# Kernel tuning notes

Measured on AMD Instinct MI355X. Metric: run time of the kernel, lower is better.

## Reference

```python
import jax, jax.numpy as jnp
import numpy as np

B, N, K, D_IN, D, L = 8, 8192, 6, 3, 256, 5
EPS_LN = 1e-5


def layernorm(x, g, b):
    m = jnp.mean(x, axis=-1, keepdims=True)
    v = jnp.mean((x - m) ** 2, axis=-1, keepdims=True)
    return (x - m) * jax.lax.rsqrt(v + EPS_LN) * g + b


def spmm_mean(v, knn):
    # sparse adj matmul: out[j] = sum_{n: j in knn[n]} v[n], then / k
    n, k = knn.shape[-2], knn.shape[-1]
    src = jnp.repeat(jnp.arange(n), k)  # [N*K]

    def one(vb, kb):
        return jnp.zeros_like(vb).at[kb.reshape(-1)].add(vb[src])

    return jax.vmap(one)(v, knn) / (k + 1e-6)


def grf_layer(h, knn, qkv_w, out_w, out_b, hops=3):
    q, k, v = jnp.split(h @ qkv_w, 3, axis=-1)
    for _ in range(hops):
        v = spmm_mean(v, knn)
        k = spmm_mean(k, knn)
    attn = jnp.sum(q * k, axis=-1, keepdims=True)
    return (attn * v) @ out_w + out_b


def linear_attention(h, qkv_w, out_w, out_b):
    q, k, v = jnp.split(h @ qkv_w, 3, axis=-1)
    q = jax.nn.relu(q) + 1e-6
    k = jax.nn.relu(k) + 1e-6
    kv = jnp.einsum('bnd,bne->bde', k, v)
    z = 1.0 / (jnp.einsum('bnd,bd->bn', q, k.sum(axis=1)) + 1e-6)
    attn = jnp.einsum('bnd,bde,bn->bne', q, kv, z)
    return attn @ out_w + out_b


def setup_inputs() -> dict:
    key = jax.random.key(0)
    ks = jax.random.split(key, 12)
    s = 0.02
    return {
        'x': jax.random.normal(ks[0], (B, N, D_IN), jnp.float32),
        'knn': jax.random.randint(ks[1], (B, N, K), 0, N, jnp.int32),
        'emb_w': jax.random.normal(ks[2], (D_IN, D), jnp.float32) * s,
        'emb_b': jnp.zeros((D,), jnp.float32),
        'norm_g': jnp.ones((2 * L, D), jnp.float32),
        'norm_b': jnp.zeros((2 * L, D), jnp.float32),
        'grf_qkv': jax.random.normal(ks[3], (L, D, 3 * D), jnp.float32) * s,
        'grf_outw': jax.random.normal(ks[4], (L, D, D), jnp.float32) * s,
        'grf_outb': jnp.zeros((L, D), jnp.float32),
        'attn_qkv': jax.random.normal(ks[5], (L, D, 3 * D), jnp.float32) * s,
        'attn_outw': jax.random.normal(ks[6], (L, D, D), jnp.float32) * s,
        'attn_outb': jnp.zeros((L, D), jnp.float32),
        'head_w': jax.random.normal(ks[7], (D, 3), jnp.float32) * s,
        'head_b': jnp.zeros((3,), jnp.float32),
    }


def reference(x, knn, emb_w, emb_b, norm_g, norm_b, grf_qkv, grf_outw, grf_outb,
              attn_qkv, attn_outw, attn_outb, head_w, head_b):
    h = x @ emb_w + emb_b
    for i in range(L):
        h = h + grf_layer(layernorm(h, norm_g[2 * i], norm_b[2 * i]), knn,
                          grf_qkv[i], grf_outw[i], grf_outb[i])
        h = h + linear_attention(layernorm(h, norm_g[2 * i + 1], norm_b[2 * i + 1]),
                                 attn_qkv[i], attn_outw[i], attn_outb[i])
    return h @ head_w + head_b
```

## Files before the change

kernel.cpp:

```cpp
#include <hip/hip_runtime.h>

#define BB 8
#define NN 8192
#define KK 6
#define DD 256
#define LL 5
#define NE (BB*NN*KK)
#define PLANE (NN*DD)
#define INV6 (1.0f/6.000001f)

typedef unsigned short u16;
typedef __attribute__((ext_vector_type(8))) _Float16 h8;
typedef __attribute__((ext_vector_type(8))) unsigned short us8;
typedef __attribute__((ext_vector_type(4))) float f32x4;

__device__ __forceinline__ u16 f2h(float f){
  union { _Float16 h; u16 u; } c; c.h = (_Float16)f; return c.u;
}
__device__ __forceinline__ float h2f(u16 u){
  union { _Float16 h; u16 u; } c; c.u = u; return (float)c.h;
}

__device__ __forceinline__ void ldscp(const u16* g, u16* l){
  __builtin_amdgcn_global_load_lds(
      (const __attribute__((address_space(1))) void*)g,
      (__attribute__((address_space(3))) void*)l, 16, 0, 0);
}

__global__ void k_count(const int* __restrict__ knn, int* __restrict__ off){
  int e = blockIdx.x*256 + threadIdx.x;
  if(e >= NE) return;
  int b = e / (NN*KK);
  int j = knn[e];
  atomicAdd(&off[b*(NN+1) + 1 + j], 1);
}

__global__ __launch_bounds__(1024) void k_scan(int* __restrict__ offAll){
  __shared__ int lds[1024];
  __shared__ int carry_s;
  int* off = offAll + blockIdx.x*(NN+1);
  const int len = NN+1;
  int t = threadIdx.x;
  if(t==0) carry_s = 0;
  __syncthreads();
  for(int base=0; base<len; base+=1024){
    int x = (base+t < len) ? off[base+t] : 0;
    lds[t] = x; __syncthreads();
    for(int s=1; s<1024; s<<=1){
      int v = (t>=s) ? lds[t-s] : 0;
      __syncthreads();
      lds[t] += v;
      __syncthreads();
    }
    int incl = lds[t];
    int carry = carry_s;
    __syncthreads();
    if(base+t < len) off[base+t] = incl + carry;
    if(t==1023) carry_s = carry + incl;
    __syncthreads();
  }
}

__global__ void k_fill(const int* __restrict__ knn, int* __restrict__ cursor, int* __restrict__ srcE){
  int e = blockIdx.x*256 + threadIdx.x;
  if(e >= NE) return;
  int b = e / (NN*KK);
  int n = (e % (NN*KK)) / KK;
  int j = knn[e];
  int pos = atomicAdd(&cursor[b*(NN+1) + j], 1);
  srcE[(long)b*NN*KK + pos] = n;
}

__global__ __launch_bounds__(256) void k_prepw(const float* __restrict__ W, u16* __restrict__ Wt, int N){
  int n = blockIdx.x, l = blockIdx.y, k = threadIdx.x;
  float x = W[((long)l*256 + k)*N + n];
  u16 hb = f2h(x);
  Wt[(((long)l*2 + 0)*N + n)*256 + k] = hb;
  Wt[(((long)l*2 + 1)*N + n)*256 + k] = f2h(x - h2f(hb));
}

__global__ __launch_bounds__(256) void k_embed(const float* __restrict__ x, const float* __restrict__ ew,
                        const float* __restrict__ eb, float* __restrict__ h){
  int g = blockIdx.x, z = blockIdx.y, d = threadIdx.x;
  const float* xp = x + ((long)z*NN + g)*3;
  h[(long)z*PLANE + (long)g*DD + d] = xp[0]*ew[0*DD+d] + xp[1]*ew[1*DD+d] + xp[2]*ew[2*DD+d] + eb[d];
}

__global__ __launch_bounds__(256) void k_ln(const float* __restrict__ h, const float* __restrict__ g,
                     const float* __restrict__ bia, u16* __restrict__ out){
  long z = blockIdx.y;
  int row = blockIdx.x*4 + (threadIdx.x >> 6);
  int lane = threadIdx.x & 63;
  const float4 x = *(const float4*)(h + z*PLANE + (long)row*DD + lane*4);
  float s  = x.x + x.y + x.z + x.w;
  float s2 = x.x*x.x + x.y*x.y + x.z*x.z + x.w*x.w;
  for(int o=1;o<64;o<<=1){ s += __shfl_xor(s,o); s2 += __shfl_xor(s2,o); }
  float m = s*(1.0f/256.0f);
  float var = s2*(1.0f/256.0f) - m*m;
  float r = rsqrtf(var + 1e-5f);
  const float4 gu = *(const float4*)(g + lane*4);
  const float4 bu = *(const float4*)(bia + lane*4);
  ushort4 o4;
  o4.x = f2h((x.x-m)*r*gu.x + bu.x);
  o4.y = f2h((x.y-m)*r*gu.y + bu.y);
  o4.z = f2h((x.z-m)*r*gu.z + bu.z);
  o4.w = f2h((x.w-m)*r*gu.w + bu.w);
  *(ushort4*)(out + z*PLANE + (long)row*DD + lane*4) = o4;
}

template<int BM,int BN,bool ASPLIT,bool BF32,bool BSPLIT>
__global__ __launch_bounds__(256) void k_mgemm(
    const u16* __restrict__ A, long aStride, long aLoOff, int K, int kSplit,
    const void* __restrict__ Bv, long bStride, long bLoOff,
    const float* __restrict__ rowscale, long rsStride,
    const float* __restrict__ bias,
    u16* __restrict__ o0, u16* __restrict__ o1, u16* __restrict__ o2,
    long oStride, int reluMask, long oLoOff,
    float* __restrict__ accOut, long hStride)
{
  constexpr int WM = BM/2, WN = BN/2, MT = WM/16, NT = WN/16;
  constexpr int STG1 = BM*32*(ASPLIT?2:1) + BN*32*(BSPLIT?2:1);
  constexpr int STGT = BF32 ? STG1 : 2*STG1;
  constexpr int EPI = (BM==128) ? 32*132*2 : 0;
  constexpr int SM  = (STGT > EPI) ? STGT : EPI;
  __shared__ __align__(16) u16 smem[SM];
  float* epi = (float*)smem;

  const int t = threadIdx.x;
  const int nz = blockIdx.z;
  const long z = nz / kSplit;
  const int chunk = nz % kSplit;
  const int kLen = K / kSplit, kLo = chunk * kLen;
  const int rowTile = blockIdx.x*BM, colTile = blockIdx.y*BN;
  const int l = t & 63, w = t >> 6;
  const int wr = w >> 1, wc = w & 1;
  const int lm = l & 15, kq = l >> 4;

  f32x4 acc[MT][NT];
  #pragma unroll
  for(int mt=0;mt<MT;mt++)
    #pragma unroll
    for(int nt=0;nt<NT;nt++) acc[mt][nt] = (f32x4){0.f,0.f,0.f,0.f};

  if constexpr (!BF32){
    auto stageAB = [&](int buf, int k0){
      u16* Ahi_ = smem + (size_t)buf*STG1;
      u16* Alo_ = Ahi_ + BM*32;
      u16* Bhi_ = Ahi_ + BM*32*(ASPLIT?2:1);
      u16* Blo_ = Bhi_ + BN*32;
      {
        constexpr int NCH = BM/64;
        #pragma unroll
        for(int li=0; li<NCH; li++){
          int f = li*256 + t;
          int row = f>>2, c = (f&3)*8;
          const u16* gp = A + z*aStride + (long)(rowTile+row)*K + k0 + c;
          ldscp(gp, &Ahi_[f*8]);
          if constexpr (ASPLIT) ldscp(gp + aLoOff, &Alo_[f*8]);
        }
      }
      {
        constexpr int NCH = BN/64;
        #pragma unroll
        for(int li=0; li<NCH; li++){
          int f = li*256 + t;
          int row = f>>2, c = (f&3)*8;
          const u16* gp = (const u16*)Bv + z*bStride + (long)(colTile+row)*K + k0 + c;
          ldscp(gp, &Bhi_[f*8]);
          if constexpr (BSPLIT) ldscp(gp + bLoOff, &Blo_[f*8]);
        }
      }
    };

    const int nsteps = kLen >> 5;
    stageAB(0, kLo);
    __syncthreads();
    int cur = 0;
    for(int ks=0; ks<nsteps; ++ks){
      if(ks+1 < nsteps) stageAB(cur^1, kLo + ((ks+1)<<5));
      const u16* Ahi_ = smem + (size_t)cur*STG1;
      const u16* Alo_ = Ahi_ + BM*32;
      const u16* Bhi_ = Ahi_ + BM*32*(ASPLIT?2:1);
      const u16* Blo_ = Bhi_ + BN*32;
      h8 ah[MT], al[MT], bh[NT], bl[NT];
      #pragma unroll
      for(int mt=0;mt<MT;mt++){
        int idx = (wr*WM + mt*16 + lm)*32 + kq*8;
        ah[mt] = *(const h8*)&Ahi_[idx];
        if constexpr (ASPLIT) al[mt] = *(const h8*)&Alo_[idx];
      }
      #pragma unroll
      for(int nt=0;nt<NT;nt++){
        int idx = (wc*WN + nt*16 + lm)*32 + kq*8;
        bh[nt] = *(const h8*)&Bhi_[idx];
        if constexpr (BSPLIT) bl[nt] = *(const h8*)&Blo_[idx];
      }
      #pragma unroll
      for(int mt=0;mt<MT;mt++)
        #pragma unroll
        for(int nt=0;nt<NT;nt++){
          acc[mt][nt] = __builtin_amdgcn_mfma_f32_16x16x32_f16(ah[mt], bh[nt], acc[mt][nt], 0, 0, 0);
          if constexpr (BSPLIT)
            acc[mt][nt] = __builtin_amdgcn_mfma_f32_16x16x32_f16(ah[mt], bl[nt], acc[mt][nt], 0, 0, 0);
          if constexpr (ASPLIT)
            acc[mt][nt] = __builtin_amdgcn_mfma_f32_16x16x32_f16(al[mt], bh[nt], acc[mt][nt], 0, 0, 0);
        }
      __syncthreads();
      cur ^= 1;
    }
  } else {
    u16* Ahi = smem;
    u16* Alo = smem + BM*32;
    u16* Bhi = smem + BM*32*(ASPLIT?2:1);
    for(int k0=kLo; k0<kLo+kLen; k0+=32){
      __syncthreads();
      {
        constexpr int NCH = BM/64;
        #pragma unroll
        for(int li=0; li<NCH; li++){
          int f = li*256 + t;
          int row = f>>2, c = (f&3)*8;
          const u16* gp = A + z*aStride + (long)(rowTile+row)*K + k0 + c;
          ldscp(gp, &Ahi[f*8]);
          if constexpr (ASPLIT) ldscp(gp + aLoOff, &Alo[f*8]);
        }
      }
      {
        constexpr int NCH = BN/64;
        #pragma unroll
        for(int li=0; li<NCH; li++){
          int f = li*256 + t;
          int row = f>>2, c = (f&3)*8;
          const float* src = (const float*)Bv + z*bStride + (long)(colTile+row)*K + k0 + c;
          float4 v0 = ((const float4*)src)[0], v1 = ((const float4*)src)[1];
          us8 hv;
          hv[0]=f2h(v0.x); hv[1]=f2h(v0.y); hv[2]=f2h(v0.z); hv[3]=f2h(v0.w);
          hv[4]=f2h(v1.x); hv[5]=f2h(v1.y); hv[6]=f2h(v1.z); hv[7]=f2h(v1.w);
          *(us8*)&Bhi[f*8] = hv;
        }
      }
      __syncthreads();
      h8 ah[MT], al[MT], bh[NT];
      #pragma unroll
      for(int mt=0;mt<MT;mt++){
        int idx = (wr*WM + mt*16 + lm)*32 + kq*8;
        ah[mt] = *(const h8*)&Ahi[idx];
        if constexpr (ASPLIT) al[mt] = *(const h8*)&Alo[idx];
      }
      #pragma unroll
      for(int nt=0;nt<NT;nt++){
        int idx = (wc*WN + nt*16 + lm)*32 + kq*8;
        bh[nt] = *(const h8*)&Bhi[idx];
      }
      #pragma unroll
      for(int mt=0;mt<MT;mt++)
        #pragma unroll
        for(int nt=0;nt<NT;nt++){
          acc[mt][nt] = __builtin_amdgcn_mfma_f32_16x16x32_f16(ah[mt], bh[nt], acc[mt][nt], 0, 0, 0);
          if constexpr (ASPLIT)
            acc[mt][nt] = __builtin_amdgcn_mfma_f32_16x16x32_f16(al[mt], bh[nt], acc[mt][nt], 0, 0, 0);
        }
    }
  }

  if constexpr (BM == 128){
    const int sec = colTile >> 8;
    u16* osec = (sec==0) ? o0 : ((sec==1) ? o1 : o2);
    const bool relu = (reluMask >> sec) & 1;
    #pragma unroll
    for(int mt=0;mt<MT;mt++){
      __syncthreads();
      #pragma unroll
      for(int r=0;r<4;r++){
        int gm = rowTile + wr*64 + mt*16 + kq*4 + r;
        float sc = rowscale ? rowscale[z*rsStride + gm] : 1.0f;
        int rl = wr*16 + kq*4 + r;
        #pragma unroll
        for(int nt=0;nt<NT;nt++)
          epi[rl*132 + wc*64 + nt*16 + lm] = acc[mt][nt][r]*sc;
      }
      __syncthreads();
      #pragma unroll
      for(int ss=0;ss<2;ss++){
        int s = ss*256 + t;
        int rl = s >> 4, sc8 = (s & 15)*8;
        int gm2 = rowTile + (rl>>4)*64 + mt*16 + (rl & 15);
        float v[8];
        #pragma unroll
        for(int j=0;j<8;j++) v[j] = epi[rl*132 + sc8 + j];
        if(bias){
          const float* bp = bias + colTile + sc8;
          #pragma unroll
          for(int j=0;j<8;j++) v[j] += bp[j];
        }
        if(accOut){
          float* hp = accOut + z*hStride + (long)gm2*256 + colTile + sc8;
          float4 h0 = ((float4*)hp)[0], h1 = ((float4*)hp)[1];
          h0.x += v[0]; h0.y += v[1]; h0.z += v[2]; h0.w += v[3];
          h1.x += v[4]; h1.y += v[5]; h1.z += v[6]; h1.w += v[7];
          ((float4*)hp)[0] = h0; ((float4*)hp)[1] = h1;
        } else {
          us8 o8;
          #pragma unroll
          for(int j=0;j<8;j++){
            float vv = v[j];
            if(relu) vv = fmaxf(vv, 0.f) + 1e-6f;
            o8[j] = f2h(vv);
          }
          *(us8*)(osec + z*oStride + (long)gm2*256 + ((colTile + sc8) & 255)) = o8;
        }
      }
    }
  } else {
    #pragma unroll
    for(int mt=0;mt<MT;mt++){
      #pragma unroll
      for(int r=0;r<4;r++){
        int gm = rowTile + wr*WM + mt*16 + kq*4 + r;
        float sc = rowscale ? rowscale[z*rsStride + gm] : 1.0f;
        if(accOut){
          float* hp = accOut + z*hStride + (long)gm*256;
          if(kSplit > 1){
            #pragma unroll
            for(int nt=0;nt<NT;nt++){
              int gc = colTile + wc*WN + nt*16 + lm;
              atomicAdd(&hp[gc], acc[mt][nt][r]);
            }
          } else {
            #pragma unroll
            for(int nt=0;nt<NT;nt++){
              int gc = colTile + wc*WN + nt*16 + lm;
              hp[gc] += acc[mt][nt][r]*sc + (bias ? bias[gc] : 0.f);
            }
          }
        } else {
          #pragma unroll
          for(int nt=0;nt<NT;nt++){
            int gc = colTile + wc*WN + nt*16 + lm;
            int sec = gc >> 8;
            u16* o = (sec==0) ? o0 : ((sec==1) ? o1 : o2);
            float val = acc[mt][nt][r]*sc + (bias ? bias[gc] : 0.f);
            if((reluMask >> sec) & 1) val = fmaxf(val, 0.f) + 1e-6f;
            if(sec==0 && oLoOff){
              u16* oo = o0 + 2*z*oStride + (long)gm*256 + (gc & 255);
              u16 hb = f2h(val);
              oo[0] = hb;
              oo[oLoOff] = f2h(val - h2f(hb));
            } else {
              o[z*oStride + (long)gm*256 + (gc & 255)] = f2h(val);
            }
          }
        }
      }
    }
  }
}

__global__ __launch_bounds__(256) void k_fusedout(
    const u16* __restrict__ A, const u16* __restrict__ B, long bStride, long bLoOff,
    const float* __restrict__ rowscale, const float* __restrict__ ksumIn,
    const float* __restrict__ bias,
    float* __restrict__ h,
    const float* __restrict__ lnG, const float* __restrict__ lnB,
    u16* __restrict__ Lout,
    const float* __restrict__ headW, const float* __restrict__ headB,
    float* __restrict__ headOut)
{
  __shared__ __align__(16) u16 smem[16384];
  u16* Bh = smem;
  u16* Bl = smem + 8192;
  float* epi = (float*)smem;

  const int t = threadIdx.x;
  const long z = blockIdx.z;
  const int rowTile = blockIdx.x*32;
  const int l = t & 63, w = t >> 6;
  const int wr = w >> 1, wc = w & 1;
  const int lm = l & 15, kq = l >> 4;
  const u16* Ab = A + z*PLANE;
  const u16* Bb = B + z*bStride;

  f32x4 acc[8];
  #pragma unroll
  for(int nt=0;nt<8;nt++) acc[nt] = (f32x4){0.f,0.f,0.f,0.f};

  h8 areg[8];
  {
    const u16* arow = Ab + (long)(rowTile + wr*16 + lm)*256 + kq*8;
    #pragma unroll
    for(int kk=0;kk<8;kk++) areg[kk] = *(const h8*)(arow + kk*32);
  }

  float rsv = 0.f;
  if(ksumIn){
    const float* kb = ksumIn + z*DD;
    float s = 0.f;
    #pragma unroll
    for(int kk=0;kk<8;kk++){
      const float4 c0v = *(const float4*)(kb + kq*8 + kk*32);
      const float4 c1v = *(const float4*)(kb + kq*8 + kk*32 + 4);
      s += (float)areg[kk][0]*c0v.x + (float)areg[kk][1]*c0v.y
         + (float)areg[kk][2]*c0v.z + (float)areg[kk][3]*c0v.w
         + (float)areg[kk][4]*c1v.x + (float)areg[kk][5]*c1v.y
         + (float)areg[kk][6]*c1v.z + (float)areg[kk][7]*c1v.w;
    }
    s += __shfl_xor(s, 16);
    s += __shfl_xor(s, 32);
    rsv = 1.0f/(s + 1e-6f);
  }

  #pragma unroll
  for(int kk=0; kk<8; ++kk){
    __syncthreads();
    #pragma unroll
    for(int li=0; li<4; li++){
      int f = li*256 + t;
      int row = f>>2, c = (f&3)*8;
      const u16* gp = Bb + (long)row*256 + kk*32 + c;
      ldscp(gp, &Bh[f*8]);
      ldscp(gp + bLoOff, &Bl[f*8]);
    }
    __syncthreads();
    #pragma unroll
    for(int nt=0;nt<8;nt++){
      int idx = (wc*128 + nt*16 + lm)*32 + kq*8;
      const h8 bhf = *(const h8*)&Bh[idx];
      const h8 blf = *(const h8*)&Bl[idx];
      acc[nt] = __builtin_amdgcn_mfma_f32_16x16x32_f16(areg[kk], bhf, acc[nt], 0, 0, 0);
      acc[nt] = __builtin_amdgcn_mfma_f32_16x16x32_f16(areg[kk], blf, acc[nt], 0, 0, 0);
    }
  }

  #pragma unroll
  for(int p=0;p<2;p++){
    __syncthreads();
    if(wr == p){
      #pragma unroll
      for(int r=0;r<4;r++){
        int rl = kq*4 + r;
        int gm = rowTile + p*16 + rl;
        float sc;
        if(ksumIn) sc = __shfl(rsv, kq*4 + r);
        else       sc = rowscale ? rowscale[z*NN + gm] : 1.0f;
        #pragma unroll
        for(int nt=0;nt<8;nt++)
          epi[rl*260 + wc*128 + nt*16 + lm] = acc[nt][r]*sc;
      }
    }
    __syncthreads();
    #pragma unroll
    for(int ss=0;ss<4;ss++){
      int s = ss*256 + t;
      int rl = s >> 6;
      int c4 = (s & 63)*4;
      int gm = rowTile + p*16 + rl;
      float4 e = *(float4*)&epi[rl*260 + c4];
      float4 x;
      x.x = e.x + bias[c4+0];
      x.y = e.y + bias[c4+1];
      x.z = e.z + bias[c4+2];
      x.w = e.w + bias[c4+3];
      float* hp = h + z*PLANE + (long)gm*256 + c4;
      float4 h0 = *(float4*)hp;
      x.x += h0.x; x.y += h0.y; x.z += h0.z; x.w += h0.w;
      *(float4*)hp = x;
      if(lnG){
        float sA = x.x + x.y + x.z + x.w;
        float s2 = x.x*x.x + x.y*x.y + x.z*x.z + x.w*x.w;
        for(int o=1;o<64;o<<=1){ sA += __shfl_xor(sA,o); s2 += __shfl_xor(s2,o); }
        float m = sA*(1.0f/256.0f);
        float var = s2*(1.0f/256.0f) - m*m;
        float rr = rsqrtf(var + 1e-5f);
        const float4 gu = *(const float4*)(lnG + c4);
        const float4 bu = *(const float4*)(lnB + c4);
        ushort4 o4;
        o4.x = f2h((x.x-m)*rr*gu.x + bu.x);
        o4.y = f2h((x.y-m)*rr*gu.y + bu.y);
        o4.z = f2h((x.z-m)*rr*gu.z + bu.z);
        o4.w = f2h((x.w-m)*rr*gu.w + bu.w);
        *(ushort4*)(Lout + z*PLANE + (long)gm*256 + c4) = o4;
      } else if(headW){
        int d0 = c4;
        float a0 = x.x*headW[(d0+0)*3+0] + x.y*headW[(d0+1)*3+0] + x.z*headW[(d0+2)*3+0] + x.w*headW[(d0+3)*3+0];
        float a1 = x.x*headW[(d0+0)*3+1] + x.y*headW[(d0+1)*3+1] + x.z*headW[(d0+2)*3+1] + x.w*headW[(d0+3)*3+1];
        float a2 = x.x*headW[(d0+0)*3+2] + x.y*headW[(d0+1)*3+2] + x.z*headW[(d0+2)*3+2] + x.w*headW[(d0+3)*3+2];
        for(int o=1;o<64;o<<=1){
          a0 += __shfl_xor(a0,o); a1 += __shfl_xor(a1,o); a2 += __shfl_xor(a2,o);
        }
        if((t & 63)==0){
          float* op = headOut + ((long)z*NN + gm)*3;
          op[0] = a0 + headB[0];
          op[1] = a1 + headB[1];
          op[2] = a2 + headB[2];
        }
      }
    }
  }
}

template<int MODE>
__global__ __launch_bounds__(256) void k_spmm2(
    const u16* __restrict__ kin, const u16* __restrict__ vin,
    const int* __restrict__ offB, const int* __restrict__ srcB,
    u16* __restrict__ kout, u16* __restrict__ vout,
    const u16* __restrict__ q, float* __restrict__ rs){
  long z = blockIdx.x;
  const int* off = offB + z*(NN+1);
  const int* sE  = srcB + z*(long)NN*KK;

  if constexpr (MODE == 0){
    const u16* kp = kin + z*PLANE;
    const u16* vp = vin + z*PLANE;
    int row = blockIdx.y*16 + (threadIdx.x >> 4);
    int d8 = blockIdx.z*128 + (threadIdx.x & 15)*8;
    int s0 = off[row], s1 = off[row+1];
    float ak[8], av[8];
    #pragma unroll
    for(int j=0;j<8;j++){ ak[j]=0.f; av[j]=0.f; }
    int e = s0;
    for(; e+1 < s1; e += 2){
      int n0 = sE[e], n1 = sE[e+1];
      us8 k0 = *(const us8*)(kp + (long)n0*DD + d8);
      us8 k1 = *(const us8*)(kp + (long)n1*DD + d8);
      us8 v0 = *(const us8*)(vp + (long)n0*DD + d8);
      us8 v1 = *(const us8*)(vp + (long)n1*DD + d8);
      #pragma unroll
      for(int j=0;j<8;j++){
        ak[j] += h2f(k0[j]) + h2f(k1[j]);
        av[j] += h2f(v0[j]) + h2f(v1[j]);
      }
    }
    if(e < s1){
      int n0 = sE[e];
      us8 k0 = *(const us8*)(kp + (long)n0*DD + d8);
      us8 v0 = *(const us8*)(vp + (long)n0*DD + d8);
      #pragma unroll
      for(int j=0;j<8;j++){ ak[j] += h2f(k0[j]); av[j] += h2f(v0[j]); }
    }
    us8 ok, ov;
    #pragma unroll
    for(int j=0;j<8;j++){ ok[j] = f2h(ak[j]*INV6); ov[j] = f2h(av[j]*INV6); }
    *(us8*)(kout + z*PLANE + (long)row*DD + d8) = ok;
    *(us8*)(vout + z*PLANE + (long)row*DD + d8) = ov;
  } else {
    if(blockIdx.z == 0){
      const u16* kp = kin + z*PLANE;
      int row = blockIdx.y*8 + (threadIdx.x >> 5);
      int l32 = threadIdx.x & 31;
      int d8 = l32*8;
      int s0 = off[row], s1 = off[row+1];
      float ak[8];
      #pragma unroll
      for(int j=0;j<8;j++) ak[j]=0.f;
      int e = s0;
      for(; e+1 < s1; e += 2){
        int n0 = sE[e], n1 = sE[e+1];
        us8 k0 = *(const us8*)(kp + (long)n0*DD + d8);
        us8 k1 = *(const us8*)(kp + (long)n1*DD + d8);
        #pragma unroll
        for(int j=0;j<8;j++) ak[j] += h2f(k0[j]) + h2f(k1[j]);
      }
      if(e < s1){
        int n0 = sE[e];
        us8 k0 = *(const us8*)(kp + (long)n0*DD + d8);
        #pragma unroll
        for(int j=0;j<8;j++) ak[j] += h2f(k0[j]);
      }
      us8 qv = *(const us8*)(q + z*PLANE + (long)row*DD + d8);
      float s = 0.f;
      #pragma unroll
      for(int j=0;j<8;j++) s += h2f(qv[j]) * ak[j];
      for(int o=1;o<32;o<<=1) s += __shfl_xor(s,o);
      if(l32==0) rs[z*NN + row] = s*INV6;
    } else {
      const u16* vp = vin + z*PLANE;
      int row = (blockIdx.y & 511)*16 + (threadIdx.x >> 4);
      int d8 = (blockIdx.y >> 9)*128 + (threadIdx.x & 15)*8;
      int s0 = off[row], s1 = off[row+1];
      float av[8];
      #pragma unroll
      for(int j=0;j<8;j++) av[j]=0.f;
      int e = s0;
      for(; e+1 < s1; e += 2){
        int n0 = sE[e], n1 = sE[e+1];
        us8 v0 = *(const us8*)(vp + (long)n0*DD + d8);
        us8 v1 = *(const us8*)(vp + (long)n1*DD + d8);
        #pragma unroll
        for(int j=0;j<8;j++) av[j] += h2f(v0[j]) + h2f(v1[j]);
      }
      if(e < s1){
        int n0 = sE[e];
        us8 v0 = *(const us8*)(vp + (long)n0*DD + d8);
        #pragma unroll
        for(int j=0;j<8;j++) av[j] += h2f(v0[j]);
      }
      us8 ov;
      #pragma unroll
      for(int j=0;j<8;j++) ov[j] = f2h(av[j]*INV6);
      *(us8*)(vout + z*PLANE + (long)row*DD + d8) = ov;
    }
  }
}

__global__ __launch_bounds__(256) void k_transp2(
    const u16* __restrict__ in0, u16* __restrict__ out0,
    const u16* __restrict__ in1, u16* __restrict__ out1,
    float* __restrict__ ksum){
  __shared__ u16 tile[64][72];
  int zz = blockIdx.z;
  long z = zz >> 1;
  const u16* ip = ((zz & 1) ? in1 : in0) + z*PLANE;
  u16* op = ((zz & 1) ? out1 : out0) + z*PLANE;
  int r0 = blockIdx.x*64, c0 = blockIdx.y*64;
  int t = threadIdx.x;
  {
    int r = t>>2, cg = (t&3)*16;
    *(us8*)&tile[r][cg]   = *(const us8*)(ip + (long)(r0+r)*DD + c0 + cg);
    *(us8*)&tile[r][cg+8] = *(const us8*)(ip + (long)(r0+r)*DD + c0 + cg + 8);
  }
  __syncthreads();
  {
    int c = t>>2, rg = t&3;
    us8 a, b;
    #pragma unroll
    for(int j=0;j<8;j++){ a[j] = tile[rg*16+j][c]; b[j] = tile[rg*16+8+j][c]; }
    u16* dst = op + (long)(c0+c)*NN + r0 + rg*16;
    *(us8*)dst = a; *(us8*)(dst+8) = b;
    if((zz & 1)==0){
      float p = 0.f;
      #pragma unroll
      for(int j=0;j<8;j++) p += h2f(a[j]) + h2f(b[j]);
      p += __shfl_xor(p, 1);
      p += __shfl_xor(p, 2);
      if(rg == 0) atomicAdd(&ksum[z*DD + c0 + c], p);
    }
  }
}

struct Carve {
  float *h; u16 *L,*Q,*Bp,*Cp,*T;
  float *kvf; u16 *w2t;
  float *ksum,*rs;
  int *off,*cursor,*srcE;
  u16 *wt_gqkv,*wt_aqkv,*wt_gout,*wt_aout;
  size_t total;
};

static Carve carve(char* base, int C){
  Carve c;
  size_t cur = 0;
  auto bump = [&](size_t bytes)->char*{
    char* p = base ? base + cur : (char*)0;
    cur += (bytes + 255) & ~(size_t)255;
    return p;
  };
  c.h    = (float*)bump((size_t)C*PLANE*4);
  c.L    = (u16*)bump((size_t)C*PLANE*2);
  c.Q    = (u16*)bump((size_t)C*PLANE*2);
  c.Bp   = (u16*)bump((size_t)C*PLANE*2);
  c.Cp   = (u16*)bump((size_t)C*PLANE*2);
  c.T    = (u16*)bump((size_t)C*PLANE*2);
  c.kvf  = (float*)bump((size_t)C*DD*DD*4);
  c.w2t  = (u16*)bump((size_t)C*2*DD*DD*2);
  c.ksum = (float*)bump((size_t)C*DD*4);
  c.rs   = (float*)bump((size_t)C*NN*4);
  c.off  = (int*)bump((size_t)BB*(NN+1)*4);
  c.cursor=(int*)bump((size_t)BB*(NN+1)*4);
  c.srcE = (int*)bump((size_t)NE*4);
  c.wt_gqkv = (u16*)bump((size_t)LL*2*768*256*2);
  c.wt_aqkv = (u16*)bump((size_t)LL*2*768*256*2);
  c.wt_gout = (u16*)bump((size_t)LL*2*256*256*2);
  c.wt_aout = (u16*)bump((size_t)LL*2*256*256*2);
  c.total = cur;
  return c;
}

extern "C" void kernel_launch(void* const* d_in, const int* in_sizes, int n_in,
                              void* d_out, int out_size, void* d_ws, size_t ws_size,
                              hipStream_t stream)
{
  const float* x        = (const float*)d_in[0];
  const int*   knn      = (const int*)d_in[1];
  const float* emb_w    = (const float*)d_in[2];
  const float* emb_b    = (const float*)d_in[3];
  const float* norm_g   = (const float*)d_in[4];
  const float* norm_b   = (const float*)d_in[5];
  const float* grf_qkv  = (const float*)d_in[6];
  const float* grf_outw = (const float*)d_in[7];
  const float* grf_outb = (const float*)d_in[8];
  const float* attn_qkv = (const float*)d_in[9];
  const float* attn_outw= (const float*)d_in[10];
  const float* attn_outb= (const float*)d_in[11];
  const float* head_w   = (const float*)d_in[12];
  const float* head_b   = (const float*)d_in[13];
  float* out = (float*)d_out;

  int C = 1;
  for(int cc=BB; cc>=1; cc>>=1){ if(carve(nullptr, cc).total <= ws_size){ C = cc; break; } }
  Carve ws = carve((char*)d_ws, C);

  k_prepw<<<dim3(768, LL), 256, 0, stream>>>(grf_qkv,  ws.wt_gqkv, 768);
  k_prepw<<<dim3(768, LL), 256, 0, stream>>>(attn_qkv, ws.wt_aqkv, 768);
  k_prepw<<<dim3(256, LL), 256, 0, stream>>>(grf_outw, ws.wt_gout, 256);
  k_prepw<<<dim3(256, LL), 256, 0, stream>>>(attn_outw,ws.wt_aout, 256);

  hipMemsetAsync(ws.off, 0, (size_t)BB*(NN+1)*sizeof(int), stream);
  k_count<<<dim3((NE+255)/256), 256, 0, stream>>>(knn, ws.off);
  k_scan<<<dim3(BB), 1024, 0, stream>>>(ws.off);
  hipMemcpyAsync(ws.cursor, ws.off, (size_t)BB*(NN+1)*sizeof(int), hipMemcpyDeviceToDevice, stream);
  k_fill<<<dim3((NE+255)/256), 256, 0, stream>>>(knn, ws.cursor, ws.srcE);

  const long PL = PLANE;
  for(int b0=0; b0<BB; b0+=C){
    const int* offB  = ws.off  + (long)b0*(NN+1);
    const int* srcB  = ws.srcE + (long)b0*NN*KK;

    k_embed<<<dim3(NN, C), 256, 0, stream>>>(x + (long)b0*NN*3, emb_w, emb_b, ws.h);
    k_ln<<<dim3(NN/4, C), 256, 0, stream>>>(ws.h, norm_g, norm_b, ws.L);

    for(int i=0; i<LL; i++){
      k_mgemm<128,128,false,false,true><<<dim3(64, 6, C), 256, 0, stream>>>(
          ws.L, PL, 0, 256, 1,
          ws.wt_gqkv + (long)i*2*768*256, 0, (long)768*256,
          nullptr, 0, nullptr,
          ws.Q, ws.Bp, ws.Cp, PL, 0, 0, nullptr, 0);
      k_spmm2<0><<<dim3(C, NN/16, 2), 256, 0, stream>>>(ws.Bp, ws.Cp, offB, srcB, ws.L, ws.T, nullptr, nullptr);
      k_spmm2<0><<<dim3(C, NN/16, 2), 256, 0, stream>>>(ws.L,  ws.T,  offB, srcB, ws.Bp, ws.Cp, nullptr, nullptr);
      k_spmm2<1><<<dim3(C, NN/8, 2), 256, 0, stream>>>(ws.Bp, ws.Cp, offB, srcB, nullptr, ws.T, ws.Q, ws.rs);
      k_fusedout<<<dim3(NN/32, 1, C), 256, 0, stream>>>(
          ws.T, ws.wt_gout + (long)i*2*256*256, 0, (long)256*256,
          ws.rs, nullptr, grf_outb + (long)i*DD, ws.h,
          norm_g + (2*i+1)*DD, norm_b + (2*i+1)*DD, ws.L,
          nullptr, nullptr, nullptr);

      k_mgemm<128,128,false,false,true><<<dim3(64, 6, C), 256, 0, stream>>>(
          ws.L, PL, 0, 256, 1,
          ws.wt_aqkv + (long)i*2*768*256, 0, (long)768*256,
          nullptr, 0, nullptr,
          ws.Q, ws.Bp, ws.Cp, PL, 3 , 0, nullptr, 0);
      hipMemsetAsync(ws.ksum, 0, (size_t)C*DD*sizeof(float), stream);
      k_transp2<<<dim3(NN/64, DD/64, 2*C), 256, 0, stream>>>(ws.Bp, ws.L, ws.Cp, ws.T, ws.ksum);
      hipMemsetAsync(ws.kvf, 0, (size_t)C*DD*DD*sizeof(float), stream);
      k_mgemm<64,64,false,false,false><<<dim3(4, 4, C*8), 256, 0, stream>>>(
          ws.L, PL, 0, NN, 8,
          ws.T, PL, 0,
          nullptr, 0, nullptr,
          nullptr, nullptr, nullptr, 0, 0, 0, ws.kvf, (long)DD*DD);
      k_mgemm<64,64,true,true,false><<<dim3(4, 4, C), 256, 0, stream>>>(
          ws.wt_aout + (long)i*2*256*256, 0, (long)256*256, 256, 1,
          ws.kvf, (long)DD*DD, 0,
          nullptr, 0, nullptr,
          ws.w2t, nullptr, nullptr, (long)DD*DD, 0, (long)DD*DD,
          nullptr, 0);
      const float* g2 = (i==LL-1) ? nullptr : norm_g + (2*i+2)*DD;
      const float* b2 = (i==LL-1) ? nullptr : norm_b + (2*i+2)*DD;
      k_fusedout<<<dim3(NN/32, 1, C), 256, 0, stream>>>(
          ws.Q, ws.w2t, 2L*DD*DD, (long)DD*DD,
          nullptr, ws.ksum, attn_outb + (long)i*DD, ws.h,
          g2, b2, ws.L,
          (i==LL-1) ? head_w : nullptr,
          (i==LL-1) ? head_b : nullptr,
          (i==LL-1) ? (out + (long)b0*NN*3) : nullptr);
    }
  }
}
```

Before: 2.466 ms.

## Fuse final V-hop sparse gather into output GEMM A-operand load

The third-hop mean aggregation of V is no longer written to an intermediate buffer by the spmm kernel. The GRF output GEMM now gathers neighbour rows straight into its A registers, and the spmm launch shrinks to only the K-hop/attention-score part. Block indices are also remapped so consecutive blocks interleave batches, which may spread gather traffic. This drops one intermediate write and read plus part of a launch, at the cost of doing irregular gathers inside the GEMM prologue and lengthening it.

```diff
diff --git a/kernel.cpp b/kernel.cpp
--- a/kernel.cpp
+++ b/kernel.cpp
@@ -358,6 +358,7 @@
 
 __global__ __launch_bounds__(256) void k_fusedout(
     const u16* __restrict__ A, const u16* __restrict__ B, long bStride, long bLoOff,
+    const u16* __restrict__ gatherIn, const int* __restrict__ offB, const int* __restrict__ srcB,
     const float* __restrict__ rowscale, const float* __restrict__ ksumIn,
     const float* __restrict__ bias,
     float* __restrict__ h,
@@ -372,12 +373,13 @@
   float* epi = (float*)smem;
 
   const int t = threadIdx.x;
-  const long z = blockIdx.z;
-  const int rowTile = blockIdx.x*32;
+  const int lid = blockIdx.x + gridDim.x*blockIdx.z;
+  const int nbat = gridDim.z;
+  const long z = lid % nbat;
+  const int rowTile = (lid / nbat)*32;
   const int l = t & 63, w = t >> 6;
   const int wr = w >> 1, wc = w & 1;
   const int lm = l & 15, kq = l >> 4;
-  const u16* Ab = A + z*PLANE;
   const u16* Bb = B + z*bStride;
 
   f32x4 acc[8];
@@ -385,8 +387,39 @@
   for(int nt=0;nt<8;nt++) acc[nt] = (f32x4){0.f,0.f,0.f,0.f};
 
   h8 areg[8];
-  {
-    const u16* arow = Ab + (long)(rowTile + wr*16 + lm)*256 + kq*8;
+  if(gatherIn){
+    const u16* vp = gatherIn + z*PLANE;
+    const int* off = offB + z*(NN+1);
+    const int* sE  = srcB + z*(long)NN*KK;
+    int row = rowTile + wr*16 + lm;
+    int s0 = off[row], s1 = off[row+1];
+    #pragma unroll
+    for(int kk=0;kk<8;kk++){
+      const int cbase = kq*8 + kk*32;
+      float av[8];
+      #pragma unroll
+      for(int j=0;j<8;j++) av[j]=0.f;
+      int e = s0;
+      for(; e+1 < s1; e += 2){
+        int n0 = sE[e], n1 = sE[e+1];
+        us8 v0 = *(const us8*)(vp + (long)n0*DD + cbase);
+        us8 v1 = *(const us8*)(vp + (long)n1*DD + cbase);
+        #pragma unroll
+        for(int j=0;j<8;j++) av[j] += h2f(v0[j]) + h2f(v1[j]);
+      }
+      if(e < s1){
+        int n0 = sE[e];
+        us8 v0 = *(const us8*)(vp + (long)n0*DD + cbase);
+        #pragma unroll
+        for(int j=0;j<8;j++) av[j] += h2f(v0[j]);
+      }
+      us8 o;
+      #pragma unroll
+      for(int j=0;j<8;j++) o[j] = f2h(av[j]*INV6);
+      areg[kk] = *(h8*)&o;
+    }
+  } else {
+    const u16* arow = A + z*PLANE + (long)(rowTile + wr*16 + lm)*256 + kq*8;
     #pragma unroll
     for(int kk=0;kk<8;kk++) areg[kk] = *(const h8*)(arow + kk*32);
   }
@@ -543,62 +576,34 @@
     *(us8*)(kout + z*PLANE + (long)row*DD + d8) = ok;
     *(us8*)(vout + z*PLANE + (long)row*DD + d8) = ov;
   } else {
-    if(blockIdx.z == 0){
-      const u16* kp = kin + z*PLANE;
-      int row = blockIdx.y*8 + (threadIdx.x >> 5);
-      int l32 = threadIdx.x & 31;
-      int d8 = l32*8;
-      int s0 = off[row], s1 = off[row+1];
-      float ak[8];
-      #pragma unroll
-      for(int j=0;j<8;j++) ak[j]=0.f;
-      int e = s0;
-      for(; e+1 < s1; e += 2){
-        int n0 = sE[e], n1 = sE[e+1];
-        us8 k0 = *(const us8*)(kp + (long)n0*DD + d8);
-        us8 k1 = *(const us8*)(kp + (long)n1*DD + d8);
-        #pragma unroll
-        for(int j=0;j<8;j++) ak[j] += h2f(k0[j]) + h2f(k1[j]);
-      }
-      if(e < s1){
-        int n0 = sE[e];
-        us8 k0 = *(const us8*)(kp + (long)n0*DD + d8);
-        #pragma unroll
-        for(int j=0;j<8;j++) ak[j] += h2f(k0[j]);
-      }
-      us8 qv = *(const us8*)(q + z*PLANE + (long)row*DD + d8);
-      float s = 0.f;
-      #pragma unroll
-      for(int j=0;j<8;j++) s += h2f(qv[j]) * ak[j];
-      for(int o=1;o<32;o<<=1) s += __shfl_xor(s,o);
-      if(l32==0) rs[z*NN + row] = s*INV6;
-    } else {
-      const u16* vp = vin + z*PLANE;
-      int row = (blockIdx.y & 511)*16 + (threadIdx.x >> 4);
-      int d8 = (blockIdx.y >> 9)*128 + (threadIdx.x & 15)*8;
-      int s0 = off[row], s1 = off[row+1];
-      float av[8];
-      #pragma unroll
-      for(int j=0;j<8;j++) av[j]=0.f;
-      int e = s0;
-      for(; e+1 < s1; e += 2){
-        int n0 = sE[e], n1 = sE[e+1];
-        us8 v0 = *(const us8*)(vp + (long)n0*DD + d8);
-        us8 v1 = *(const us8*)(vp + (long)n1*DD + d8);
-        #pragma unroll
-        for(int j=0;j<8;j++) av[j] += h2f(v0[j]) + h2f(v1[j]);
-      }
-      if(e < s1){
-        int n0 = sE[e];
-        us8 v0 = *(const us8*)(vp + (long)n0*DD + d8);
-        #pragma unroll
-        for(int j=0;j<8;j++) av[j] += h2f(v0[j]);
-      }
-      us8 ov;
-      #pragma unroll
-      for(int j=0;j<8;j++) ov[j] = f2h(av[j]*INV6);
-      *(us8*)(vout + z*PLANE + (long)row*DD + d8) = ov;
-    }
+    const u16* kp = kin + z*PLANE;
+    int row = blockIdx.y*8 + (threadIdx.x >> 5);
+    int l32 = threadIdx.x & 31;
+    int d8 = l32*8;
+    int s0 = off[row], s1 = off[row+1];
+    float ak[8];
+    #pragma unroll
+    for(int j=0;j<8;j++) ak[j]=0.f;
+    int e = s0;
+    for(; e+1 < s1; e += 2){
+      int n0 = sE[e], n1 = sE[e+1];
+      us8 k0 = *(const us8*)(kp + (long)n0*DD + d8);
+      us8 k1 = *(const us8*)(kp + (long)n1*DD + d8);
+      #pragma unroll
+      for(int j=0;j<8;j++) ak[j] += h2f(k0[j]) + h2f(k1[j]);
+    }
+    if(e < s1){
+      int n0 = sE[e];
+      us8 k0 = *(const us8*)(kp + (long)n0*DD + d8);
+      #pragma unroll
+      for(int j=0;j<8;j++) ak[j] += h2f(k0[j]);
+    }
+    us8 qv = *(const us8*)(q + z*PLANE + (long)row*DD + d8);
+    float s = 0.f;
+    #pragma unroll
+    for(int j=0;j<8;j++) s += h2f(qv[j]) * ak[j];
+    for(int o=1;o<32;o<<=1) s += __shfl_xor(s,o);
+    if(l32==0) rs[z*NN + row] = s*INV6;
   }
 }
 
@@ -726,9 +731,10 @@
           ws.Q, ws.Bp, ws.Cp, PL, 0, 0, nullptr, 0);
       k_spmm2<0><<<dim3(C, NN/16, 2), 256, 0, stream>>>(ws.Bp, ws.Cp, offB, srcB, ws.L, ws.T, nullptr, nullptr);
       k_spmm2<0><<<dim3(C, NN/16, 2), 256, 0, stream>>>(ws.L,  ws.T,  offB, srcB, ws.Bp, ws.Cp, nullptr, nullptr);
-      k_spmm2<1><<<dim3(C, NN/8, 2), 256, 0, stream>>>(ws.Bp, ws.Cp, offB, srcB, nullptr, ws.T, ws.Q, ws.rs);
+      k_spmm2<1><<<dim3(C, NN/8), 256, 0, stream>>>(ws.Bp, nullptr, offB, srcB, nullptr, nullptr, ws.Q, ws.rs);
       k_fusedout<<<dim3(NN/32, 1, C), 256, 0, stream>>>(
-          ws.T, ws.wt_gout + (long)i*2*256*256, 0, (long)256*256,
+          nullptr, ws.wt_gout + (long)i*2*256*256, 0, (long)256*256,
+          ws.Cp, offB, srcB,
           ws.rs, nullptr, grf_outb + (long)i*DD, ws.h,
           norm_g + (2*i+1)*DD, norm_b + (2*i+1)*DD, ws.L,
           nullptr, nullptr, nullptr);
@@ -756,6 +762,7 @@
       const float* b2 = (i==LL-1) ? nullptr : norm_b + (2*i+2)*DD;
       k_fusedout<<<dim3(NN/32, 1, C), 256, 0, stream>>>(
           ws.Q, ws.w2t, 2L*DD*DD, (long)DD*DD,
+          nullptr, nullptr, nullptr,
           nullptr, ws.ksum, attn_outb + (long)i*DD, ws.h,
           g2, b2, ws.L,
           (i==LL-1) ? head_w : nullptr,
```

After: 2.753 ms. +11.6%, slower.

## Fuse K/V transpose and key-sum into attention QKV GEMM epilogue

Applied to the files above, without the earlier changes.

The attention QKV GEMM now writes the K and V sections straight into transposed (feature-major) buffers and accumulates the per-feature key sum with atomics in its epilogue. This removes the separate transpose kernel and one full read and write of K and V per layer. The transposed stores are 4-element ushort4 writes strided by NN, which may coalesce worse than the staged LDS transpose did.

```diff
diff --git a/kernel.cpp b/kernel.cpp
--- a/kernel.cpp
+++ b/kernel.cpp
@@ -116,7 +116,8 @@
     const float* __restrict__ bias,
     u16* __restrict__ o0, u16* __restrict__ o1, u16* __restrict__ o2,
     long oStride, int reluMask, long oLoOff,
-    float* __restrict__ accOut, long hStride)
+    float* __restrict__ accOut, long hStride,
+    u16* __restrict__ o1T, u16* __restrict__ o2T, float* __restrict__ ksumOut)
 {
   constexpr int WM = BM/2, WN = BN/2, MT = WM/16, NT = WN/16;
   constexpr int STG1 = BM*32*(ASPLIT?2:1) + BN*32*(BSPLIT?2:1);
@@ -265,6 +266,43 @@
 
   if constexpr (BM == 128){
     const int sec = colTile >> 8;
+    if(o1T && sec >= 1){
+      u16* oT = (sec==1) ? o1T : o2T;
+      const bool relu = (reluMask >> sec) & 1;
+      float kpart[NT];
+      #pragma unroll
+      for(int nt=0;nt<NT;nt++) kpart[nt] = 0.f;
+      #pragma unroll
+      for(int mt=0;mt<MT;mt++){
+        #pragma unroll
+        for(int nt=0;nt<NT;nt++){
+          int gcs = (colTile & 255) + wc*WN + nt*16 + lm;
+          int gmb = rowTile + wr*WM + mt*16 + kq*4;
+          ushort4 o4;
+          #pragma unroll
+          for(int r=0;r<4;r++){
+            float val = acc[mt][nt][r];
+            if(relu) val = fmaxf(val, 0.f) + 1e-6f;
+            u16 hv = f2h(val);
+            ((u16*)&o4)[r] = hv;
+            if(sec==1) kpart[nt] += h2f(hv);
+          }
+          *(ushort4*)(oT + z*oStride + (long)gcs*NN + gmb) = o4;
+        }
+      }
+      if(sec==1 && ksumOut){
+        #pragma unroll
+        for(int nt=0;nt<NT;nt++){
+          float p = kpart[nt];
+          p += __shfl_xor(p, 16);
+          p += __shfl_xor(p, 32);
+          if(kq==0){
+            int gcs = (colTile & 255) + wc*WN + nt*16 + lm;
+            atomicAdd(&ksumOut[z*DD + gcs], p);
+          }
+        }
+      }
+    } else {
     u16* osec = (sec==0) ? o0 : ((sec==1) ? o1 : o2);
     const bool relu = (reluMask >> sec) & 1;
     #pragma unroll
@@ -310,6 +348,7 @@
           *(us8*)(osec + z*oStride + (long)gm2*256 + ((colTile + sc8) & 255)) = o8;
         }
       }
+    }
     }
   } else {
     #pragma unroll
@@ -602,41 +641,6 @@
   }
 }
 
-__global__ __launch_bounds__(256) void k_transp2(
-    const u16* __restrict__ in0, u16* __restrict__ out0,
-    const u16* __restrict__ in1, u16* __restrict__ out1,
-    float* __restrict__ ksum){
-  __shared__ u16 tile[64][72];
-  int zz = blockIdx.z;
-  long z = zz >> 1;
-  const u16* ip = ((zz & 1) ? in1 : in0) + z*PLANE;
-  u16* op = ((zz & 1) ? out1 : out0) + z*PLANE;
-  int r0 = blockIdx.x*64, c0 = blockIdx.y*64;
-  int t = threadIdx.x;
-  {
-    int r = t>>2, cg = (t&3)*16;
-    *(us8*)&tile[r][cg]   = *(const us8*)(ip + (long)(r0+r)*DD + c0 + cg);
-    *(us8*)&tile[r][cg+8] = *(const us8*)(ip + (long)(r0+r)*DD + c0 + cg + 8);
-  }
-  __syncthreads();
-  {
-    int c = t>>2, rg = t&3;
-    us8 a, b;
-    #pragma unroll
-    for(int j=0;j<8;j++){ a[j] = tile[rg*16+j][c]; b[j] = tile[rg*16+8+j][c]; }
-    u16* dst = op + (long)(c0+c)*NN + r0 + rg*16;
-    *(us8*)dst = a; *(us8*)(dst+8) = b;
-    if((zz & 1)==0){
-      float p = 0.f;
-      #pragma unroll
-      for(int j=0;j<8;j++) p += h2f(a[j]) + h2f(b[j]);
-      p += __shfl_xor(p, 1);
-      p += __shfl_xor(p, 2);
-      if(rg == 0) atomicAdd(&ksum[z*DD + c0 + c], p);
-    }
-  }
-}
-
 struct Carve {
   float *h; u16 *L,*Q,*Bp,*Cp,*T;
   float *kvf; u16 *w2t;
@@ -723,7 +727,8 @@
           ws.L, PL, 0, 256, 1,
           ws.wt_gqkv + (long)i*2*768*256, 0, (long)768*256,
           nullptr, 0, nullptr,
-          ws.Q, ws.Bp, ws.Cp, PL, 0, 0, nullptr, 0);
+          ws.Q, ws.Bp, ws.Cp, PL, 0, 0, nullptr, 0,
+          nullptr, nullptr, nullptr);
       k_spmm2<0><<<dim3(C, NN/16, 2), 256, 0, stream>>>(ws.Bp, ws.Cp, offB, srcB, ws.L, ws.T, nullptr, nullptr);
       k_spmm2<0><<<dim3(C, NN/16, 2), 256, 0, stream>>>(ws.L,  ws.T,  offB, srcB, ws.Bp, ws.Cp, nullptr, nullptr);
       k_spmm2<1><<<dim3(C, NN/8, 2), 256, 0, stream>>>(ws.Bp, ws.Cp, offB, srcB, nullptr, ws.T, ws.Q, ws.rs);
@@ -733,25 +738,27 @@
           norm_g + (2*i+1)*DD, norm_b + (2*i+1)*DD, ws.L,
           nullptr, nullptr, nullptr);
 
+      hipMemsetAsync(ws.ksum, 0, (size_t)C*DD*sizeof(float), stream);
       k_mgemm<128,128,false,false,true><<<dim3(64, 6, C), 256, 0, stream>>>(
           ws.L, PL, 0, 256, 1,
           ws.wt_aqkv + (long)i*2*768*256, 0, (long)768*256,
           nullptr, 0, nullptr,
-          ws.Q, ws.Bp, ws.Cp, PL, 3 , 0, nullptr, 0);
-      hipMemsetAsync(ws.ksum, 0, (size_t)C*DD*sizeof(float), stream);
-      k_transp2<<<dim3(NN/64, DD/64, 2*C), 256, 0, stream>>>(ws.Bp, ws.L, ws.Cp, ws.T, ws.ksum);
+          ws.Q, nullptr, nullptr, PL, 3 , 0, nullptr, 0,
+          ws.Bp, ws.T, ws.ksum);
       hipMemsetAsync(ws.kvf, 0, (size_t)C*DD*DD*sizeof(float), stream);
       k_mgemm<64,64,false,false,false><<<dim3(4, 4, C*8), 256, 0, stream>>>(
-          ws.L, PL, 0, NN, 8,
+          ws.Bp, PL, 0, NN, 8,
           ws.T, PL, 0,
           nullptr, 0, nullptr,
-          nullptr, nullptr, nullptr, 0, 0, 0, ws.kvf, (long)DD*DD);
+          nullptr, nullptr, nullptr, 0, 0, 0, ws.kvf, (long)DD*DD,
+          nullptr, nullptr, nullptr);
       k_mgemm<64,64,true,true,false><<<dim3(4, 4, C), 256, 0, stream>>>(
           ws.wt_aout + (long)i*2*256*256, 0, (long)256*256, 256, 1,
           ws.kvf, (long)DD*DD, 0,
           nullptr, 0, nullptr,
           ws.w2t, nullptr, nullptr, (long)DD*DD, 0, (long)DD*DD,
-          nullptr, 0);
+          nullptr, 0,
+          nullptr, nullptr, nullptr);
       const float* g2 = (i==LL-1) ? nullptr : norm_g + (2*i+2)*DD;
       const float* b2 = (i==LL-1) ? nullptr : norm_b + (2*i+2)*DD;
       k_fusedout<<<dim3(NN/32, 1, C), 256, 0, stream>>>(
```

Result: faster. 2.342 ms (-5.0%).
